# Kernel tuning notes

Hardware: AMD Instinct MI355X
Metric: run time of the kernel (lower is better)

The kernel has to match this reference:

```python
import jax, jax.numpy as jnp
import numpy as np

TEMPERATURE_F = 0.5


def setup_inputs() -> dict:
    key = jax.random.key(0)
    k1, k2, k3, k4, k5 = jax.random.split(key, 5)
    B, D, K = 4096, 128, 8192
    return {
        "h_i": jax.random.normal(k1, (B, D), dtype=jnp.float32),
        "h_j": jax.random.normal(k2, (B, D), dtype=jnp.float32),
        "sub_graph": jax.random.uniform(k3, (B, K), dtype=jnp.float32),
        "sub_x": jax.random.normal(k4, (B, D), dtype=jnp.float32),
        "all_x": jax.random.normal(k5, (K, D), dtype=jnp.float32),
    }


def _forward_feature(h_i, h_j):
    # NT-Xent contrastive loss (CrossEntropyLoss with label 0, reduction='sum', /N).
    B = h_i.shape[0]
    N = 2 * B
    h = jnp.concatenate([h_i, h_j], axis=0)           # [N, D]
    sim = (h @ h.T) / TEMPERATURE_F                   # [N, N]
    idx = jnp.arange(N)
    pos = sim[idx, (idx + B) % N]                     # positives: diag(sim, +B) ++ diag(sim, -B)
    # logits row i = [pos_i] ++ {sim[i,j] : j != i, j != i±B}. Since pos_i == sim[i, i±B],
    # the logsumexp over that row equals logsumexp over sim[i,:] with only the diagonal removed.
    sim_nodiag = jnp.where(jnp.eye(N, dtype=bool), -jnp.inf, sim)
    lse = jax.nn.logsumexp(sim_nodiag, axis=1)        # [N]
    return jnp.sum(lse - pos) / N


def _graph_loss(sub_graph, sub_x, all_x):
    # trace(X^T diag(r) X) = sum_i r_i * ||X_i||^2 ; trace(A^T G B) = sum(G * (A B^T)) = sum((G B) * A)
    r = jnp.sum(sub_graph, axis=1)                    # [M]
    c = jnp.sum(sub_graph, axis=0)                    # [K]
    t1 = jnp.sum(r * jnp.sum(sub_x * sub_x, axis=1))
    t2 = jnp.sum(c * jnp.sum(all_x * all_x, axis=1))
    t3 = jnp.sum((sub_graph @ all_x) * sub_x)         # trace(sub_x^T G all_x)
    M, K = sub_graph.shape
    return (t1 + t2 - 2.0 * t3) / (M * K)


def reference(h_i, h_j, sub_graph, sub_x, all_x):
    contrastive = _forward_feature(h_i, h_j)
    graph = _graph_loss(sub_graph, sub_x, all_x)
    return contrastive + graph
```

## Files before the change

### kernel.cpp

```cpp
#include <hip/hip_runtime.h>
#include <hip/hip_bf16.h>

typedef __attribute__((ext_vector_type(4)))  float f32x4;
typedef __attribute__((ext_vector_type(16))) float f32x16;
typedef __attribute__((ext_vector_type(8)))  short s16x8;
typedef unsigned short u16;
typedef unsigned int u32;

#define ALPHA 1.6986436f
#define LN2F  0.69314718056f
#define COFF  128.0f

__device__ __forceinline__ u16 f2bf(float x) {
  union { float f; u32 u; } v; v.f = x;
  u32 r = v.u + 0x7fffu + ((v.u >> 16) & 1u);
  return (u16)(r >> 16);
}

#if __has_builtin(__builtin_amdgcn_exp2f)
__device__ __forceinline__ float fexp2(float x) { return __builtin_amdgcn_exp2f(x); }
#else
__device__ __forceinline__ float fexp2(float x) { return exp2f(x); }
#endif
#if __has_builtin(__builtin_amdgcn_logf)
__device__ __forceinline__ float flog2(float x) { return __builtin_amdgcn_logf(x); }
#else
__device__ __forceinline__ float flog2(float x) { return log2f(x); }
#endif

__device__ __forceinline__ s16x8 cvt8(float4 a, float4 b) {
  union { u32 w[4]; s16x8 v; } u;
  asm("v_cvt_pk_bf16_f32 %0, %1, %2" : "=v"(u.w[0]) : "v"(a.x), "v"(a.y));
  asm("v_cvt_pk_bf16_f32 %0, %1, %2" : "=v"(u.w[1]) : "v"(a.z), "v"(a.w));
  asm("v_cvt_pk_bf16_f32 %0, %1, %2" : "=v"(u.w[2]) : "v"(b.x), "v"(b.y));
  asm("v_cvt_pk_bf16_f32 %0, %1, %2" : "=v"(u.w[3]) : "v"(b.z), "v"(b.w));
  return u.v;
}

__device__ __forceinline__ f32x16 mfma32(s16x8 a, s16x8 b, f32x16 c) {
  return __builtin_amdgcn_mfma_f32_32x32x16_bf16(a, b, c, 0, 0, 0);
}
__device__ __forceinline__ f32x16 zero16() {
  f32x16 z;
#pragma unroll
  for (int i = 0; i < 16; ++i) z[i] = 0.f;
  return z;
}
__device__ __forceinline__ void gl16(const void* g, void* l) {
  __builtin_amdgcn_global_load_lds(
      (const __attribute__((address_space(1))) u32*)g,
      (__attribute__((address_space(3))) u32*)l, 16, 0, 0);
}

__global__ __launch_bounds__(256)
void prep_all(const float* __restrict__ h_i, const float* __restrict__ h_j,
              const float* __restrict__ all_x, const float* __restrict__ subx,
              u16* __restrict__ hbf, u16* __restrict__ axG,
              float* __restrict__ nall, float* __restrict__ nsub,
              float* __restrict__ pos4) {
  __shared__ float tile[64 * 132];
  int bid = blockIdx.x, tid = threadIdx.x;
  if (bid < 512) {
    int t = bid * 256 + tid;
    int row = t >> 4, kb = t & 15;
    const float* src = (row < 4096 ? h_i + (size_t)row * 128
                                   : h_j + (size_t)(row - 4096) * 128) + kb * 8;
    float4 f0 = *(const float4*)(src);
    float4 f1 = *(const float4*)(src + 4);
    float4 sa = {ALPHA * f0.x, ALPHA * f0.y, ALPHA * f0.z, ALPHA * f0.w};
    float4 sb = {ALPHA * f1.x, ALPHA * f1.y, ALPHA * f1.z, ALPHA * f1.w};
    s16x8 o = cvt8(sa, sb);
    char* dst = (char*)hbf + (size_t)row * 256 + ((kb * 16) ^ ((row & 7) << 4));
    *(s16x8*)dst = o;
    if (row < 4096) {
      const float* srcj = h_j + (size_t)row * 128 + kb * 8;
      float4 g0 = *(const float4*)(srcj);
      float4 g1 = *(const float4*)(srcj + 4);
      float dp = f0.x * g0.x + f0.y * g0.y + f0.z * g0.z + f0.w * g0.w
               + f1.x * g1.x + f1.y * g1.y + f1.z * g1.z + f1.w * g1.w;
      dp += __shfl_xor(dp, 1, 64);
      dp += __shfl_xor(dp, 2, 64);
      dp += __shfl_xor(dp, 4, 64);
      dp += __shfl_xor(dp, 8, 64);
      if ((tid & 15) == 0) pos4[row] = 2.0f * dp;
    }
  } else if (bid < 640) {
    int ab = bid - 512;
    int k0 = ab * 64;
#pragma unroll
    for (int j = 0; j < 8; ++j) {
      int idx = (j * 256 + tid) * 4;
      int kk = idx >> 7, d = idx & 127;
      *(float4*)&tile[kk * 132 + d] = *(const float4*)&all_x[(size_t)(k0 + kk) * 128 + d];
    }
    __syncthreads();
    {
      int kk = tid >> 2, q = tid & 3;
      float s = 0.f;
#pragma unroll
      for (int dd = 0; dd < 32; ++dd) { float v = tile[kk * 132 + q * 32 + dd]; s += v * v; }
      s += __shfl_xor(s, 1, 64);
      s += __shfl_xor(s, 2, 64);
      if (q == 0) nall[k0 + kk] = s;
    }
#pragma unroll
    for (int half = 0; half < 2; ++half) {
      int tgt = half * 256 + tid;
      int f = tgt >> 7, d = tgt & 127;
      int kc = ab * 4 + f;
      u16* dp = axG + (size_t)kc * 2048 + d * 16;
      s16x8 o0, o1;
#pragma unroll
      for (int kk = 0; kk < 8; ++kk) {
        o0[kk] = (short)f2bf(tile[(f * 16 + kk) * 132 + d]);
        o1[kk] = (short)f2bf(tile[(f * 16 + 8 + kk) * 132 + d]);
      }
      ((s16x8*)dp)[0] = o0; ((s16x8*)dp)[1] = o1;
    }
  } else {
    int i = (bid - 640) * 256 + tid;
    const float* p = subx + (size_t)i * 128;
    float s = 0.f;
#pragma unroll
    for (int c = 0; c < 32; ++c) {
      float4 v = ((const float4*)p)[c];
      s += v.x * v.x + v.y * v.y + v.z * v.z + v.w * v.w;
    }
    nsub[i] = s;
  }
}

__global__ __launch_bounds__(256, 3)
void main_fused(const float* __restrict__ G, const float* __restrict__ subx,
                const u16* __restrict__ axG, const float* __restrict__ nall,
                const float* __restrict__ nsub, const u16* __restrict__ hbf,
                float* __restrict__ spart, float* __restrict__ gpart) {
  __shared__ char pool[16640];
  int bid = blockIdx.x, tid = threadIdx.x;
  int lane = tid & 63, w = tid >> 6, il = lane & 31, hi = lane >> 5;

  if ((bid & 1) == 0) {
    int gid = bid >> 1;
    int mt = gid >> 3, kq = gid & 7;
    int i0 = mt * 32;
    int kbase = kq * 1024;
    int srow = tid >> 3, s8 = tid & 7;
    u16 (*gtile)[32][64] = (u16(*)[32][64])pool;
    float* nll  = (float*)(pool + 8192);
    float* wsum = (float*)(pool + 12288);
    const float* gsrc = G + (size_t)(i0 + srow) * 8192 + kbase + s8 * 4;
    int sw_w = (srow & 7) << 4;
    int wo0 = ((s8 << 3))      ^ sw_w;
    int wo1 = (64 | (s8 << 3)) ^ sw_w;
    char* wb0 = (char*)&gtile[0][srow][0];
    char* wb1 = (char*)&gtile[1][srow][0];
    int swr = (il & 7) << 4;
    const char* aBase = (const char*)axG + (size_t)(kq * 64) * 4096
                      + (size_t)w * 1024 + il * 32 + hi * 16;

    *(float4*)&nll[tid * 4] = *(const float4*)&nall[kbase + tid * 4];
    __syncthreads();

    f32x16 acc = zero16();
    float rsum = 0.f, nsum = 0.f;
    float4 gA0, gB0, gA1, gB1;

#define GISSUE(S, GA, GB)                                              \
    { const float* p_ = gsrc + (S) * 64;                               \
      GA = *(const float4*)p_; GB = *(const float4*)(p_ + 32); }

#define GCOMMIT(GA, GB, DSTB, SC)                                                  \
    { u32 c0_, c1_, c2_, c3_;                                                      \
      asm("v_cvt_pk_bf16_f32 %0, %1, %2" : "=v"(c0_) : "v"(GA.x), "v"(GA.y));      \
      asm("v_cvt_pk_bf16_f32 %0, %1, %2" : "=v"(c1_) : "v"(GA.z), "v"(GA.w));      \
      asm("v_cvt_pk_bf16_f32 %0, %1, %2" : "=v"(c2_) : "v"(GB.x), "v"(GB.y));      \
      asm("v_cvt_pk_bf16_f32 %0, %1, %2" : "=v"(c3_) : "v"(GB.z), "v"(GB.w));      \
      *(uint2*)((DSTB) + wo0) = make_uint2(c0_, c1_);                              \
      *(uint2*)((DSTB) + wo1) = make_uint2(c2_, c3_);                              \
      float4 NA = *(const float4*)&nll[(SC) * 64 + s8 * 4];                        \
      float4 NB = *(const float4*)&nll[(SC) * 64 + s8 * 4 + 32];                   \
      rsum += GA.x + GA.y + GA.z + GA.w + GB.x + GB.y + GB.z + GB.w;               \
      nsum += GA.x * NA.x + GA.y * NA.y + GA.z * NA.z + GA.w * NA.w                \
            + GB.x * NB.x + GB.y * NB.y + GB.z * NB.z + GB.w * NB.w; }

#define GBAR()                                                \
    asm volatile("s_waitcnt lgkmcnt(0)" ::: "memory");        \
    __builtin_amdgcn_sched_barrier(0);                        \
    __builtin_amdgcn_s_barrier();                             \
    __builtin_amdgcn_sched_barrier(0);

#define GSTEP(S, GA_I, GB_I, GA_O, GB_O, CURB, OTHB)                               \
    { const char* aB_ = aBase + (size_t)((S) * 4) * 4096;                          \
      s16x8 aF0 = *(const s16x8*)(aB_);                                            \
      s16x8 aF1 = *(const s16x8*)(aB_ + 4096);                                     \
      s16x8 aF2 = *(const s16x8*)(aB_ + 8192);                                     \
      s16x8 aF3 = *(const s16x8*)(aB_ + 12288);                                    \
      if ((S) < 14) GISSUE((S) + 2, GA_I, GB_I);                                   \
      const char* rb_ = (const char*)&gtile[CURB][il][0];                          \
      s16x8 B0 = *(const s16x8*)(rb_ + ((0 * 32 + hi * 16) ^ swr));                \
      s16x8 B1 = *(const s16x8*)(rb_ + ((1 * 32 + hi * 16) ^ swr));                \
      s16x8 B2 = *(const s16x8*)(rb_ + ((2 * 32 + hi * 16) ^ swr));                \
      s16x8 B3 = *(const s16x8*)(rb_ + ((3 * 32 + hi * 16) ^ swr));                \
      acc = mfma32(aF0, B0, acc);                                                  \
      acc = mfma32(aF1, B1, acc);                                                  \
      acc = mfma32(aF2, B2, acc);                                                  \
      acc = mfma32(aF3, B3, acc);                                                  \
      if ((S) < 15) GCOMMIT(GA_O, GB_O, (OTHB), (S) + 1);                          \
      GBAR(); }

    GISSUE(0, gA0, gB0);
    GISSUE(1, gA1, gB1);
    GCOMMIT(gA0, gB0, wb0, 0);
    GBAR();
    for (int sp = 0; sp < 8; ++sp) {
      int s = sp * 2;
      GSTEP(s,     gA0, gB0, gA1, gB1, 0, wb1);
      GSTEP(s + 1, gA1, gB1, gA0, gB0, 1, wb0);
    }
#undef GSTEP
#undef GBAR
#undef GCOMMIT
#undef GISSUE

    float p = rsum * nsub[i0 + srow] + nsum;
    const float* sxr = subx + (size_t)(i0 + il) * 128 + w * 32 + hi * 4;
#pragma unroll
    for (int rq = 0; rq < 4; ++rq) {
      float4 sx = *(const float4*)(sxr + rq * 8);
      p -= 2.0f * (acc[rq * 4 + 0] * sx.x + acc[rq * 4 + 1] * sx.y +
                   acc[rq * 4 + 2] * sx.z + acc[rq * 4 + 3] * sx.w);
    }
#pragma unroll
    for (int d = 1; d < 64; d <<= 1) p += __shfl_xor(p, d, 64);
    if (lane == 0) wsum[w] = p;
    __syncthreads();
    if (tid == 0) gpart[gid] = wsum[0] + wsum[1] + wsum[2] + wsum[3];
  } else {
    int cid = bid >> 1;
    int rt = cid >> 5, oct = cid & 31;
    int C0 = oct * 256;
    int rowbase = rt * 256 + w * 64;
    char (*clds)[8192] = (char(*)[8192])pool;
    s16x8 bf0[8], bf1[8];
#pragma unroll
    for (int rs = 0; rs < 2; ++rs) {
      int r = rowbase + rs * 32 + il;
      const char* rp = (const char*)hbf + (size_t)r * 256;
      int sw = (r & 7) << 4;
#pragma unroll
      for (int ks = 0; ks < 8; ++ks) {
        s16x8 v = *(const s16x8*)(rp + ((ks * 32 + hi * 16) ^ sw));
        if (rs == 0) bf0[ks] = v; else bf1[ks] = v;
      }
    }
    float s0 = 0.f, s1 = 0.f;
    auto stage = [&](int buf, int t) {
      const char* src = (const char*)hbf + (size_t)(C0 + t * 32) * 256 + tid * 16;
      char* dst = &clds[buf][0] + tid * 16;
      gl16(src, dst);
      gl16(src + 4096, dst + 4096);
    };
    stage(0, 0);
    __syncthreads();
    int cur = 0;
    for (int t = 0; t < 8; ++t) {
      if (t < 7) stage(cur ^ 1, t + 1);
      const char* basep = &clds[cur][0];
      s16x8 af[8];
#pragma unroll
      for (int ks = 0; ks < 8; ++ks)
        af[ks] = *(const s16x8*)(basep + il * 256 + ((ks * 32 + hi * 16) ^ ((il & 7) << 4)));
      f32x16 A0 = zero16(), A1 = zero16();
#pragma unroll
      for (int ks = 0; ks < 8; ++ks) {
        A0 = mfma32(af[ks], bf0[ks], A0);
        A1 = mfma32(af[ks], bf1[ks], A1);
      }
      int cb = C0 + t * 32;
      bool d0 = (cb == rowbase), d1 = (cb == rowbase + 32);
      if (!(d0 | d1)) {
#pragma unroll
        for (int r = 0; r < 16; ++r) {
          s0 += fexp2(A0[r] - COFF);
          s1 += fexp2(A1[r] - COFF);
        }
      } else {
#pragma unroll
        for (int r = 0; r < 16; ++r) {
          int jc = (r & 3) + 8 * (r >> 2) + 4 * hi;
          float t0 = fexp2(A0[r] - COFF);
          float t1 = fexp2(A1[r] - COFF);
          if (d0 && jc == il) t0 = 0.f;
          if (d1 && jc == il) t1 = 0.f;
          s0 += t0; s1 += t1;
        }
      }
      __syncthreads();
      cur ^= 1;
    }
    s0 += __shfl_xor(s0, 32, 64);
    s1 += __shfl_xor(s1, 32, 64);
    if (hi == 0) {
      spart[oct * 8192 + rowbase + il]      = s0;
      spart[oct * 8192 + rowbase + 32 + il] = s1;
    }
  }
}

__global__ __launch_bounds__(256)
void epilogue1(const float* __restrict__ spart, const float* __restrict__ pos4,
               float* __restrict__ cpart) {
  int tid = threadIdx.x;
  int row = blockIdx.x * 256 + tid;
  float S = 0.f;
#pragma unroll
  for (int o = 0; o < 32; ++o) S += spart[o * 8192 + row];
  float c = LN2F * (COFF + flog2(S)) - pos4[row & 4095];
#pragma unroll
  for (int d = 1; d < 64; d <<= 1) c += __shfl_xor(c, d, 64);
  __shared__ float ws4[4];
  int l = tid & 63, w = tid >> 6;
  if (l == 0) ws4[w] = c;
  __syncthreads();
  if (tid == 0) cpart[blockIdx.x] = ws4[0] + ws4[1] + ws4[2] + ws4[3];
}

__global__ __launch_bounds__(256)
void final_sum(const float* __restrict__ cpart, const float* __restrict__ gpart,
               float* __restrict__ out) {
  int tid = threadIdx.x;
  double gd = 0.0;
  for (int idx = tid; idx < 1024; idx += 256) gd += (double)gpart[idx];
  double cd = (tid < 32) ? (double)cpart[tid] : 0.0;
#pragma unroll
  for (int d = 1; d < 64; d <<= 1) {
    cd += __shfl_xor(cd, d, 64);
    gd += __shfl_xor(gd, d, 64);
  }
  __shared__ double wc[4], wg[4];
  int l = tid & 63, w = tid >> 6;
  if (l == 0) { wc[w] = cd; wg[w] = gd; }
  __syncthreads();
  if (tid == 0) {
    double C = wc[0] + wc[1] + wc[2] + wc[3];
    double Gs = wg[0] + wg[1] + wg[2] + wg[3];
    out[0] = (float)(C / 8192.0 + Gs / (4096.0 * 8192.0));
  }
}

extern "C" void kernel_launch(void* const* d_in, const int* in_sizes, int n_in,
                              void* d_out, int out_size, void* d_ws, size_t ws_size,
                              hipStream_t stream) {
  const float* h_i = (const float*)d_in[0];
  const float* h_j = (const float*)d_in[1];
  const float* G   = (const float*)d_in[2];
  const float* sx  = (const float*)d_in[3];
  const float* ax  = (const float*)d_in[4];
  char* ws = (char*)d_ws;
  u16*   hbf   = (u16*)(ws);
  u16*   axG   = (u16*)(ws + 2097152);
  float* nall  = (float*)(ws + 4194304);
  float* nsub  = (float*)(ws + 4227072);
  float* pos4  = (float*)(ws + 4243456);
  float* spart = (float*)(ws + 4259840);
  float* gpart = (float*)(ws + 5308416);
  float* cpart = (float*)(ws + 5312512);
  float* out = (float*)d_out;

  prep_all<<<dim3(656), dim3(256), 0, stream>>>(h_i, h_j, ax, sx, hbf, axG, nall, nsub, pos4);
  main_fused<<<dim3(2048), dim3(256), 0, stream>>>(G, sx, axG, nall, nsub, hbf, spart, gpart);
  epilogue1<<<dim3(32), dim3(256), 0, stream>>>(spart, pos4, cpart);
  final_sum<<<dim3(1), dim3(256), 0, stream>>>(cpart, gpart, out);
}
```

Before: 61.89 us.

## Restructure graph-loss blocks so each wave owns an independent tile without block barriers

New measurement: 66.53 us. 1.07x slower.

```diff
diff --git a/kernel.cpp b/kernel.cpp
--- a/kernel.cpp
+++ b/kernel.cpp
@@ -130,113 +130,111 @@
   }
 }
 
-__global__ __launch_bounds__(256, 3)
+__global__ __launch_bounds__(256, 2)
 void main_fused(const float* __restrict__ G, const float* __restrict__ subx,
                 const u16* __restrict__ axG, const float* __restrict__ nall,
                 const float* __restrict__ nsub, const u16* __restrict__ hbf,
                 float* __restrict__ spart, float* __restrict__ gpart) {
-  __shared__ char pool[16640];
+  __shared__ char pool[32768];
   int bid = blockIdx.x, tid = threadIdx.x;
   int lane = tid & 63, w = tid >> 6, il = lane & 31, hi = lane >> 5;
-
-  if ((bid & 1) == 0) {
-    int gid = bid >> 1;
-    int mt = gid >> 3, kq = gid & 7;
+  int base = bid / 3, q = bid - base * 3;
+
+  if (q == 0) {
+    int task = base * 4 + w;
+    int mt = task >> 4, kq = task & 15;
     int i0 = mt * 32;
-    int kbase = kq * 1024;
-    int srow = tid >> 3, s8 = tid & 7;
-    u16 (*gtile)[32][64] = (u16(*)[32][64])pool;
-    float* nll  = (float*)(pool + 8192);
-    float* wsum = (float*)(pool + 12288);
-    const float* gsrc = G + (size_t)(i0 + srow) * 8192 + kbase + s8 * 4;
-    int sw_w = (srow & 7) << 4;
-    int wo0 = ((s8 << 3))      ^ sw_w;
-    int wo1 = (64 | (s8 << 3)) ^ sw_w;
-    char* wb0 = (char*)&gtile[0][srow][0];
-    char* wb1 = (char*)&gtile[1][srow][0];
-    int swr = (il & 7) << 4;
-    const char* aBase = (const char*)axG + (size_t)(kq * 64) * 4096
-                      + (size_t)w * 1024 + il * 32 + hi * 16;
-
-    *(float4*)&nll[tid * 4] = *(const float4*)&nall[kbase + tid * 4];
-    __syncthreads();
-
-    f32x16 acc = zero16();
-    float rsum = 0.f, nsum = 0.f;
-    float4 gA0, gB0, gA1, gB1;
-
-#define GISSUE(S, GA, GB)                                              \
-    { const float* p_ = gsrc + (S) * 64;                               \
-      GA = *(const float4*)p_; GB = *(const float4*)(p_ + 32); }
-
-#define GCOMMIT(GA, GB, DSTB, SC)                                                  \
-    { u32 c0_, c1_, c2_, c3_;                                                      \
-      asm("v_cvt_pk_bf16_f32 %0, %1, %2" : "=v"(c0_) : "v"(GA.x), "v"(GA.y));      \
-      asm("v_cvt_pk_bf16_f32 %0, %1, %2" : "=v"(c1_) : "v"(GA.z), "v"(GA.w));      \
-      asm("v_cvt_pk_bf16_f32 %0, %1, %2" : "=v"(c2_) : "v"(GB.x), "v"(GB.y));      \
-      asm("v_cvt_pk_bf16_f32 %0, %1, %2" : "=v"(c3_) : "v"(GB.z), "v"(GB.w));      \
-      *(uint2*)((DSTB) + wo0) = make_uint2(c0_, c1_);                              \
-      *(uint2*)((DSTB) + wo1) = make_uint2(c2_, c3_);                              \
-      float4 NA = *(const float4*)&nll[(SC) * 64 + s8 * 4];                        \
-      float4 NB = *(const float4*)&nll[(SC) * 64 + s8 * 4 + 32];                   \
-      rsum += GA.x + GA.y + GA.z + GA.w + GB.x + GB.y + GB.z + GB.w;               \
-      nsum += GA.x * NA.x + GA.y * NA.y + GA.z * NA.z + GA.w * NA.w                \
-            + GB.x * NB.x + GB.y * NB.y + GB.z * NB.z + GB.w * NB.w; }
-
-#define GBAR()                                                \
-    asm volatile("s_waitcnt lgkmcnt(0)" ::: "memory");        \
-    __builtin_amdgcn_sched_barrier(0);                        \
-    __builtin_amdgcn_s_barrier();                             \
+    int kt0 = kq * 512;
+    int sr = lane >> 4, sc = lane & 15;
+    const float* gws = G + (size_t)(i0 + sr) * 8192 + kt0 + sc * 4;
+    const float* nws = nall + kt0 + sc * 4;
+    char* buf0 = pool + w * 8192;
+    char* buf1 = buf0 + 4096;
+    const char* aBase = (const char*)axG + (size_t)(kq * 32) * 4096
+                      + il * 32 + hi * 16;
+
+    float nsb[8];
+#pragma unroll
+    for (int j = 0; j < 8; ++j) nsb[j] = nsub[i0 + sr + j * 4];
+
+    f32x16 acc[4];
+#pragma unroll
+    for (int t = 0; t < 4; ++t) acc[t] = zero16();
+    float p1 = 0.f, p2 = 0.f;
+    float4 gr1[8], gr2[8];
+    float4 na1, na2;
+
+    auto gi = [&](int s, float4* gr, float4& na) {
+#pragma unroll
+      for (int j = 0; j < 8; ++j)
+        gr[j] = *(const float4*)(gws + (size_t)j * 32768 + s * 64);
+      na = *(const float4*)(nws + s * 64);
+    };
+    auto gc = [&](const float4* gr, const float4& na, char* buf) {
+#pragma unroll
+      for (int j = 0; j < 8; ++j) {
+        float4 g = gr[j];
+        u32 c0, c1;
+        asm("v_cvt_pk_bf16_f32 %0, %1, %2" : "=v"(c0) : "v"(g.x), "v"(g.y));
+        asm("v_cvt_pk_bf16_f32 %0, %1, %2" : "=v"(c1) : "v"(g.z), "v"(g.w));
+        int r = sr + j * 4;
+        *(uint2*)(buf + r * 128 + ((sc * 8) ^ ((r & 7) << 4))) = make_uint2(c0, c1);
+        p1 += (g.x + g.y + g.z + g.w) * nsb[j];
+        p2 += g.x * na.x + g.y * na.y + g.z * na.z + g.w * na.w;
+      }
+    };
+
+    gi(0, gr1, na1);
+    gc(gr1, na1, buf0);
+    gi(1, gr1, na1);
+    gi(2, gr2, na2);
+    asm volatile("s_waitcnt lgkmcnt(0)" ::: "memory");
     __builtin_amdgcn_sched_barrier(0);
 
-#define GSTEP(S, GA_I, GB_I, GA_O, GB_O, CURB, OTHB)                               \
-    { const char* aB_ = aBase + (size_t)((S) * 4) * 4096;                          \
-      s16x8 aF0 = *(const s16x8*)(aB_);                                            \
-      s16x8 aF1 = *(const s16x8*)(aB_ + 4096);                                     \
-      s16x8 aF2 = *(const s16x8*)(aB_ + 8192);                                     \
-      s16x8 aF3 = *(const s16x8*)(aB_ + 12288);                                    \
-      if ((S) < 14) GISSUE((S) + 2, GA_I, GB_I);                                   \
-      const char* rb_ = (const char*)&gtile[CURB][il][0];                          \
-      s16x8 B0 = *(const s16x8*)(rb_ + ((0 * 32 + hi * 16) ^ swr));                \
-      s16x8 B1 = *(const s16x8*)(rb_ + ((1 * 32 + hi * 16) ^ swr));                \
-      s16x8 B2 = *(const s16x8*)(rb_ + ((2 * 32 + hi * 16) ^ swr));                \
-      s16x8 B3 = *(const s16x8*)(rb_ + ((3 * 32 + hi * 16) ^ swr));                \
-      acc = mfma32(aF0, B0, acc);                                                  \
-      acc = mfma32(aF1, B1, acc);                                                  \
-      acc = mfma32(aF2, B2, acc);                                                  \
-      acc = mfma32(aF3, B3, acc);                                                  \
-      if ((S) < 15) GCOMMIT(GA_O, GB_O, (OTHB), (S) + 1);                          \
-      GBAR(); }
-
-    GISSUE(0, gA0, gB0);
-    GISSUE(1, gA1, gB1);
-    GCOMMIT(gA0, gB0, wb0, 0);
-    GBAR();
-    for (int sp = 0; sp < 8; ++sp) {
-      int s = sp * 2;
-      GSTEP(s,     gA0, gB0, gA1, gB1, 0, wb1);
-      GSTEP(s + 1, gA1, gB1, gA0, gB0, 1, wb0);
-    }
-#undef GSTEP
-#undef GBAR
-#undef GCOMMIT
-#undef GISSUE
-
-    float p = rsum * nsub[i0 + srow] + nsum;
-    const float* sxr = subx + (size_t)(i0 + il) * 128 + w * 32 + hi * 4;
-#pragma unroll
-    for (int rq = 0; rq < 4; ++rq) {
-      float4 sx = *(const float4*)(sxr + rq * 8);
-      p -= 2.0f * (acc[rq * 4 + 0] * sx.x + acc[rq * 4 + 1] * sx.y +
-                   acc[rq * 4 + 2] * sx.z + acc[rq * 4 + 3] * sx.w);
+#pragma unroll
+    for (int s = 0; s < 8; ++s) {
+      char* rb = (s & 1) ? buf1 : buf0;
+      char* wb = (s & 1) ? buf0 : buf1;
+      int swz = (il & 7) << 4;
+      s16x8 B0 = *(const s16x8*)(rb + il * 128 + ((0  + hi * 16) ^ swz));
+      s16x8 B1 = *(const s16x8*)(rb + il * 128 + ((32 + hi * 16) ^ swz));
+      s16x8 B2 = *(const s16x8*)(rb + il * 128 + ((64 + hi * 16) ^ swz));
+      s16x8 B3 = *(const s16x8*)(rb + il * 128 + ((96 + hi * 16) ^ swz));
+#pragma unroll
+      for (int kc4 = 0; kc4 < 4; ++kc4) {
+        const char* ab = aBase + (size_t)(s * 4 + kc4) * 4096;
+        s16x8 A0 = *(const s16x8*)(ab);
+        s16x8 A1 = *(const s16x8*)(ab + 1024);
+        s16x8 A2 = *(const s16x8*)(ab + 2048);
+        s16x8 A3 = *(const s16x8*)(ab + 3072);
+        s16x8 Bk = (kc4 == 0) ? B0 : (kc4 == 1) ? B1 : (kc4 == 2) ? B2 : B3;
+        acc[0] = mfma32(A0, Bk, acc[0]);
+        acc[1] = mfma32(A1, Bk, acc[1]);
+        acc[2] = mfma32(A2, Bk, acc[2]);
+        acc[3] = mfma32(A3, Bk, acc[3]);
+      }
+      if (s < 7) { if (s & 1) gc(gr2, na2, wb); else gc(gr1, na1, wb); }
+      if (s < 5) { if (s & 1) gi(s + 3, gr2, na2); else gi(s + 3, gr1, na1); }
+      asm volatile("s_waitcnt lgkmcnt(0)" ::: "memory");
+      __builtin_amdgcn_sched_barrier(0);
+    }
+
+    float p = p1 + p2;
+#pragma unroll
+    for (int t = 0; t < 4; ++t) {
+      const float* sxr = subx + (size_t)(i0 + il) * 128 + t * 32 + hi * 4;
+#pragma unroll
+      for (int rq = 0; rq < 4; ++rq) {
+        float4 sx = *(const float4*)(sxr + rq * 8);
+        p -= 2.0f * (acc[t][rq * 4 + 0] * sx.x + acc[t][rq * 4 + 1] * sx.y +
+                     acc[t][rq * 4 + 2] * sx.z + acc[t][rq * 4 + 3] * sx.w);
+      }
     }
 #pragma unroll
     for (int d = 1; d < 64; d <<= 1) p += __shfl_xor(p, d, 64);
-    if (lane == 0) wsum[w] = p;
-    __syncthreads();
-    if (tid == 0) gpart[gid] = wsum[0] + wsum[1] + wsum[2] + wsum[3];
+    if (lane == 0) gpart[task] = p;
   } else {
-    int cid = bid >> 1;
+    int cid = base * 2 + (q - 1);
     int rt = cid >> 5, oct = cid & 31;
     int C0 = oct * 256;
     int rowbase = rt * 256 + w * 64;
@@ -330,7 +328,7 @@
                float* __restrict__ out) {
   int tid = threadIdx.x;
   double gd = 0.0;
-  for (int idx = tid; idx < 1024; idx += 256) gd += (double)gpart[idx];
+  for (int idx = tid; idx < 2048; idx += 256) gd += (double)gpart[idx];
   double cd = (tid < 32) ? (double)cpart[tid] : 0.0;
 #pragma unroll
   for (int d = 1; d < 64; d <<= 1) {
@@ -364,11 +362,11 @@
   float* pos4  = (float*)(ws + 4243456);
   float* spart = (float*)(ws + 4259840);
   float* gpart = (float*)(ws + 5308416);
-  float* cpart = (float*)(ws + 5312512);
+  float* cpart = (float*)(ws + 5316608);
   float* out = (float*)d_out;
 
   prep_all<<<dim3(656), dim3(256), 0, stream>>>(h_i, h_j, ax, sx, hbf, axG, nall, nsub, pos4);
-  main_fused<<<dim3(2048), dim3(256), 0, stream>>>(G, sx, axG, nall, nsub, hbf, spart, gpart);
+  main_fused<<<dim3(1536), dim3(256), 0, stream>>>(G, sx, axG, nall, nsub, hbf, spart, gpart);
   epilogue1<<<dim3(32), dim3(256), 0, stream>>>(spart, pos4, cpart);
   final_sum<<<dim3(1), dim3(256), 0, stream>>>(cpart, gpart, out);
 }
```
